# Kernel tuning notes

Hardware: AMD Instinct MI355X
Metric: run time of the kernel (lower is better)

Reference implementation:

```python
import jax, jax.numpy as jnp
import numpy as np
import math

IN_CH = 256
RED_CH = 32  # max(256//8, 32)

def setup_inputs() -> dict:
    key = jax.random.key(0)
    k1, k2, k3, k4, k5 = jax.random.split(key, 5)
    x = jax.random.normal(k1, (2, IN_CH, 8, 28, 28), dtype=jnp.float32)
    # 1x1x1 Conv3d weights, kaiming-normal style scale (fan_out)
    def kaiming(k, shape):
        fan_out = shape[0]
        std = math.sqrt(2.0 / fan_out)
        return jax.random.normal(k, shape, dtype=jnp.float32) * std
    q_w = kaiming(k2, (RED_CH, IN_CH))
    k_w = kaiming(k3, (RED_CH, IN_CH))
    v_w = kaiming(k4, (RED_CH, IN_CH))
    out_w = kaiming(k5, (IN_CH, RED_CH))
    return {"x": x, "q_w": q_w, "k_w": k_w, "v_w": v_w, "out_w": out_w}

def reference(x, q_w, k_w, v_w, out_w):
    b, c, t, h, w = x.shape
    n = t * h * w
    xf = x.reshape(b, c, n)  # [B, C, N] (1x1x1 conv == channel matmul)
    q = jnp.einsum('rc,bcn->brn', q_w, xf)  # [B, Cr, N]
    k = jnp.einsum('rc,bcn->brn', k_w, xf)
    v = jnp.einsum('rc,bcn->brn', v_w, xf)
    scale = 1.0 / math.sqrt(RED_CH)
    attn = jnp.einsum('bri,brj->bij', q, k) * scale  # [B, N, N]
    attn = jax.nn.softmax(attn, axis=2)
    out = jnp.einsum('brj,bij->bri', v, attn)  # [B, Cr, N]
    out = jnp.einsum('cr,brn->bcn', out_w, out).reshape(b, c, t, h, w)
    return x + out
```

## Files before the change

kernel.cpp:

```cpp
#include <hip/hip_runtime.h>
#include <hip/hip_bf16.h>

#define NPOS 6272
#define NT   98
#define CIN  256
#define CR   32
#define BATCH 2
#define QS2  0.25503371989518595f
#define PPITCH 72

typedef short bf16x8s __attribute__((ext_vector_type(8)));
typedef short short4v __attribute__((ext_vector_type(4)));
typedef float f32x4   __attribute__((ext_vector_type(4)));
typedef unsigned short ushort_t;

__device__ __forceinline__ ushort_t f2bf(float f) {
    unsigned u = __builtin_bit_cast(unsigned, f);
    u += 0x7fff + ((u >> 16) & 1);
    return (ushort_t)(u >> 16);
}
__device__ __forceinline__ float bf2f(ushort_t h) {
    return __builtin_bit_cast(float, (unsigned)h << 16);
}

__global__ __launch_bounds__(256) void qkv_kernel(
    const float* __restrict__ x, const float* __restrict__ qw,
    const float* __restrict__ kw, const float* __restrict__ vw,
    ushort_t* __restrict__ Qh, ushort_t* __restrict__ Ql,
    ushort_t* __restrict__ Kh, ushort_t* __restrict__ Kl,
    ushort_t* __restrict__ Vt)
{
    const int b   = blockIdx.y;
    const int z   = blockIdx.z;
    const int nl  = threadIdx.x & 63;
    const int n   = blockIdx.x * 64 + nl;
    const int g   = __builtin_amdgcn_readfirstlane(threadIdx.x >> 6);
    const float* w  = (z == 0) ? qw : (z == 1) ? kw : vw;
    const float* xb = x + (size_t)b * CIN * NPOS + n;

    float acc[8];
#pragma unroll
    for (int i = 0; i < 8; ++i) acc[i] = 0.f;
#pragma unroll 8
    for (int c = 0; c < CIN; ++c) {
        float xv = xb[(size_t)c * NPOS];
#pragma unroll
        for (int i = 0; i < 8; ++i)
            acc[i] += w[(g * 8 + i) * CIN + c] * xv;
    }
    if (z == 2) {
#pragma unroll
        for (int i = 0; i < 8; ++i)
            Vt[((size_t)b * CR + g * 8 + i) * NPOS + n] = f2bf(acc[i]);
    } else {
        ushort_t* dh = (z == 0) ? Qh : Kh;
        ushort_t* dl = (z == 0) ? Ql : Kl;
        float s = (z == 0) ? QS2 : 1.0f;
        bf16x8s fh, fl;
#pragma unroll
        for (int i = 0; i < 8; ++i) {
            float v = acc[i] * s;
            ushort_t h = f2bf(v);
            fh[i] = (short)h;
            fl[i] = (short)f2bf(v - bf2f(h));
        }
        size_t off = ((size_t)b * NPOS + n) * CR + g * 8;
        *(bf16x8s*)(dh + off) = fh;
        *(bf16x8s*)(dl + off) = fl;
    }
}

__device__ __forceinline__ void load_tile(
    const ushort_t* __restrict__ Khb, const ushort_t* __restrict__ Klb,
    const ushort_t* __restrict__ Vtb, int j0, int col, int quad,
    bf16x8s* kh, bf16x8s* kl, bf16x8s* vb)
{
#pragma unroll
    for (int f = 0; f < 4; ++f) {
        kh[f] = *(const bf16x8s*)(Khb + (size_t)(j0 + f * 16 + col) * CR + quad * 8);
        kl[f] = *(const bf16x8s*)(Klb + (size_t)(j0 + f * 16 + col) * CR + quad * 8);
    }
#pragma unroll
    for (int k2 = 0; k2 < 2; ++k2)
#pragma unroll
        for (int c = 0; c < 2; ++c)
            vb[k2 * 2 + c] = *(const bf16x8s*)(
                Vtb + (size_t)(c * 16 + col) * NPOS + j0 + k2 * 32 + quad * 8);
}

__device__ __forceinline__ void compute_tile(
    const bf16x8s* kh, const bf16x8s* kl, const bf16x8s* vb,
    const bf16x8s* qbh, const bf16x8s* qbl,
    f32x4 (&oc)[2][2], float (&m_)[2], float (&l_)[2],
    ushort_t* pb, int col, int quad)
{
    f32x4 z4 = {0.f, 0.f, 0.f, 0.f};
#pragma unroll
    for (int h = 0; h < 2; ++h) {
        f32x4 sc[4];
#pragma unroll
        for (int f = 0; f < 4; ++f) {
            sc[f] = __builtin_amdgcn_mfma_f32_16x16x32_bf16(kl[f], qbh[h], z4, 0, 0, 0);
            sc[f] = __builtin_amdgcn_mfma_f32_16x16x32_bf16(kh[f], qbl[h], sc[f], 0, 0, 0);
            sc[f] = __builtin_amdgcn_mfma_f32_16x16x32_bf16(kh[f], qbh[h], sc[f], 0, 0, 0);
        }
        float v0 = fmaxf(fmaxf(sc[0][0], sc[0][1]), fmaxf(sc[0][2], sc[0][3]));
        float v1 = fmaxf(fmaxf(sc[1][0], sc[1][1]), fmaxf(sc[1][2], sc[1][3]));
        float v2 = fmaxf(fmaxf(sc[2][0], sc[2][1]), fmaxf(sc[2][2], sc[2][3]));
        float v3 = fmaxf(fmaxf(sc[3][0], sc[3][1]), fmaxf(sc[3][2], sc[3][3]));
        float v  = fmaxf(fmaxf(v0, v1), fmaxf(v2, v3));
        v = fmaxf(v, __shfl_xor(v, 16));
        v = fmaxf(v, __shfl_xor(v, 32));
        float mo = m_[h];
        float mn = fmaxf(mo, v);
        float al = __builtin_amdgcn_exp2f(mo - mn);
        float lsum = 0.f;
#pragma unroll
        for (int f = 0; f < 4; ++f) {
            float p0 = __builtin_amdgcn_exp2f(sc[f][0] - mn);
            float p1 = __builtin_amdgcn_exp2f(sc[f][1] - mn);
            float p2 = __builtin_amdgcn_exp2f(sc[f][2] - mn);
            float p3 = __builtin_amdgcn_exp2f(sc[f][3] - mn);
            lsum += (p0 + p1) + (p2 + p3);
            short4v pk;
            pk[0] = (short)f2bf(p0); pk[1] = (short)f2bf(p1);
            pk[2] = (short)f2bf(p2); pk[3] = (short)f2bf(p3);
            *(short4v*)(&pb[h * 16 * PPITCH + col * PPITCH + f * 16 + quad * 4]) = pk;
        }
        m_[h] = mn;
        l_[h] = l_[h] * al + lsum;
#pragma unroll
        for (int r = 0; r < 4; ++r) { oc[h][0][r] *= al; oc[h][1][r] *= al; }
    }
#pragma unroll
    for (int h = 0; h < 2; ++h) {
#pragma unroll
        for (int k2 = 0; k2 < 2; ++k2) {
            bf16x8s pbo = *(const bf16x8s*)(
                &pb[h * 16 * PPITCH + col * PPITCH + k2 * 32 + quad * 8]);
            oc[h][0] = __builtin_amdgcn_mfma_f32_16x16x32_bf16(vb[k2 * 2 + 0], pbo, oc[h][0], 0, 0, 0);
            oc[h][1] = __builtin_amdgcn_mfma_f32_16x16x32_bf16(vb[k2 * 2 + 1], pbo, oc[h][1], 0, 0, 0);
        }
    }
}

template <int ITERS>
__global__ __launch_bounds__(128, 2) void attn_kernel(
    const ushort_t* __restrict__ Qh, const ushort_t* __restrict__ Ql,
    const ushort_t* __restrict__ Kh, const ushort_t* __restrict__ Kl,
    const ushort_t* __restrict__ Vt, ushort_t* __restrict__ Opart,
    float* __restrict__ Mp, float* __restrict__ Lp)
{
    __shared__ __align__(16) ushort_t pbuf[2 * 2 * 16 * PPITCH];

    const int lane = threadIdx.x & 63;
    const int wv   = threadIdx.x >> 6;
    const int col  = lane & 15;
    const int quad = lane >> 4;
    const int b    = blockIdx.z;
    const int s    = blockIdx.y;
    const int qw0  = blockIdx.x * 64 + wv * 32;
    ushort_t* pb   = &pbuf[wv * 2 * 16 * PPITCH];

    const ushort_t* Qhb = Qh + (size_t)b * NPOS * CR;
    const ushort_t* Qlb = Ql + (size_t)b * NPOS * CR;
    const ushort_t* Khb = Kh + (size_t)b * NPOS * CR;
    const ushort_t* Klb = Kl + (size_t)b * NPOS * CR;
    const ushort_t* Vtb = Vt + (size_t)b * CR * NPOS;

    bf16x8s qbh[2], qbl[2];
    qbh[0] = *(const bf16x8s*)(Qhb + (size_t)(qw0 + col) * CR + quad * 8);
    qbh[1] = *(const bf16x8s*)(Qhb + (size_t)(qw0 + 16 + col) * CR + quad * 8);
    qbl[0] = *(const bf16x8s*)(Qlb + (size_t)(qw0 + col) * CR + quad * 8);
    qbl[1] = *(const bf16x8s*)(Qlb + (size_t)(qw0 + 16 + col) * CR + quad * 8);

    f32x4 oc[2][2];
#pragma unroll
    for (int h = 0; h < 2; ++h)
#pragma unroll
        for (int c = 0; c < 2; ++c)
#pragma unroll
            for (int r = 0; r < 4; ++r) oc[h][c][r] = 0.f;
    float m_[2] = { -1e30f, -1e30f };
    float l_[2] = { 0.f, 0.f };

    if constexpr (ITERS <= 14) {
        bf16x8s ckh[4], ckl[4], cvb[4], nkh[4], nkl[4], nvb[4];
        load_tile(Khb, Klb, Vtb, s * ITERS * 64, col, quad, ckh, ckl, cvb);
#pragma unroll
        for (int it = 0; it < ITERS; ++it) {
            if (it + 1 < ITERS)
                load_tile(Khb, Klb, Vtb, (s * ITERS + it + 1) * 64, col, quad,
                          nkh, nkl, nvb);
            compute_tile(ckh, ckl, cvb, qbh, qbl, oc, m_, l_, pb, col, quad);
            if (it + 1 < ITERS) {
#pragma unroll
                for (int f = 0; f < 4; ++f) {
                    ckh[f] = nkh[f]; ckl[f] = nkl[f]; cvb[f] = nvb[f];
                }
            }
        }
    } else {
        for (int it = 0; it < ITERS; ++it) {
            bf16x8s kh[4], kl[4], vb[4];
            load_tile(Khb, Klb, Vtb, (s * ITERS + it) * 64, col, quad, kh, kl, vb);
            compute_tile(kh, kl, vb, qbh, qbl, oc, m_, l_, pb, col, quad);
        }
    }

#pragma unroll
    for (int h = 0; h < 2; ++h) {
        float l = l_[h];
        l += __shfl_xor(l, 16);
        l += __shfl_xor(l, 32);
        l_[h] = l;
    }

    const size_t sb = (size_t)(s * BATCH + b);
    ushort_t* Ob = Opart + sb * CR * NPOS;
#pragma unroll
    for (int h = 0; h < 2; ++h)
#pragma unroll
        for (int c = 0; c < 2; ++c)
#pragma unroll
            for (int r = 0; r < 4; ++r) {
                int ch = c * 16 + quad * 4 + r;
                Ob[(size_t)ch * NPOS + qw0 + h * 16 + col] = f2bf(oc[h][c][r]);
            }
    if (quad == 0) {
#pragma unroll
        for (int h = 0; h < 2; ++h) {
            Mp[sb * NPOS + qw0 + h * 16 + col] = m_[h];
            Lp[sb * NPOS + qw0 + h * 16 + col] = l_[h];
        }
    }
}

template <int S_>
__global__ __launch_bounds__(256) void merge_kernel(
    const ushort_t* __restrict__ Opart, const float* __restrict__ Mp,
    const float* __restrict__ Lp, float* __restrict__ Omrg)
{
    const int b  = blockIdx.y;
    const int z  = blockIdx.z;
    const int nl = threadIdx.x & 63;
    const int n  = blockIdx.x * 64 + nl;
    const int g  = __builtin_amdgcn_readfirstlane(threadIdx.x >> 6);
    const int r  = z * 4 + g;

    float mg = -1e30f;
#pragma unroll
    for (int s = 0; s < S_; ++s)
        mg = fmaxf(mg, Mp[(size_t)(s * BATCH + b) * NPOS + n]);
    float lg = 0.f, acc = 0.f;
#pragma unroll
    for (int s = 0; s < S_; ++s) {
        size_t sb = (size_t)(s * BATCH + b);
        float w = __builtin_amdgcn_exp2f(Mp[sb * NPOS + n] - mg);
        lg  += w * Lp[sb * NPOS + n];
        acc += w * bf2f(Opart[(sb * CR + r) * NPOS + n]);
    }
    Omrg[((size_t)b * CR + r) * NPOS + n] = acc / lg;
}

__global__ __launch_bounds__(256) void proj_kernel(
    const float* __restrict__ Omrg, const float* __restrict__ ow,
    const float* __restrict__ x, float* __restrict__ y)
{
    const int b  = blockIdx.y;
    const int z  = blockIdx.z;
    const int nl = threadIdx.x & 63;
    const int n  = blockIdx.x * 64 + nl;
    const int g  = __builtin_amdgcn_readfirstlane(threadIdx.x >> 6);

    float o[CR];
#pragma unroll
    for (int r = 0; r < CR; ++r)
        o[r] = Omrg[((size_t)b * CR + r) * NPOS + n];

    const float* xb = x + (size_t)b * CIN * NPOS + n;
    float*       yb = y + (size_t)b * CIN * NPOS + n;
    const int c0 = z * 32 + g * 8;
#pragma unroll
    for (int cc = 0; cc < 8; ++cc) {
        int c = c0 + cc;
        float acc = xb[(size_t)c * NPOS];
#pragma unroll
        for (int r = 0; r < CR; ++r) acc += ow[c * CR + r] * o[r];
        yb[(size_t)c * NPOS] = acc;
    }
}

extern "C" void kernel_launch(void* const* d_in, const int* in_sizes, int n_in,
                              void* d_out, int out_size, void* d_ws, size_t ws_size,
                              hipStream_t stream)
{
    const float* x  = (const float*)d_in[0];
    const float* qw = (const float*)d_in[1];
    const float* kw = (const float*)d_in[2];
    const float* vw = (const float*)d_in[3];
    const float* ow = (const float*)d_in[4];
    float* out = (float*)d_out;

    const size_t qkvN = (size_t)BATCH * CR * NPOS;
    const int s_cand[4] = {14, 7, 2, 1};
    int S = 1;
    for (int i = 0; i < 4; ++i) {
        int Sc = s_cand[i];
        size_t need = 5 * qkvN * sizeof(ushort_t)
                    + qkvN * sizeof(float)
                    + (size_t)Sc * qkvN * sizeof(ushort_t)
                    + 2 * (size_t)Sc * BATCH * NPOS * sizeof(float);
        if (need <= ws_size) { S = Sc; break; }
    }
    ushort_t* Qh = (ushort_t*)d_ws;
    ushort_t* Ql = Qh + qkvN;
    ushort_t* Kh = Ql + qkvN;
    ushort_t* Kl = Kh + qkvN;
    ushort_t* Vt = Kl + qkvN;
    float* Omrg  = (float*)(Vt + qkvN);
    ushort_t* Op = (ushort_t*)(Omrg + qkvN);
    float* Mp    = (float*)(Op + (size_t)S * qkvN);
    float* Lp    = Mp + (size_t)S * BATCH * NPOS;

    qkv_kernel<<<dim3(NT, BATCH, 3), 256, 0, stream>>>(x, qw, kw, vw,
                                                       Qh, Ql, Kh, Kl, Vt);
    dim3 ag(NT, S, BATCH);
    switch (S) {
        case 14: attn_kernel<7> <<<ag, 128, 0, stream>>>(Qh, Ql, Kh, Kl, Vt, Op, Mp, Lp); break;
        case 7:  attn_kernel<14><<<ag, 128, 0, stream>>>(Qh, Ql, Kh, Kl, Vt, Op, Mp, Lp); break;
        case 2:  attn_kernel<49><<<ag, 128, 0, stream>>>(Qh, Ql, Kh, Kl, Vt, Op, Mp, Lp); break;
        default: attn_kernel<98><<<ag, 128, 0, stream>>>(Qh, Ql, Kh, Kl, Vt, Op, Mp, Lp); break;
    }
    dim3 mg(NT, BATCH, 8);
    switch (S) {
        case 14: merge_kernel<14><<<mg, 256, 0, stream>>>(Op, Mp, Lp, Omrg); break;
        case 7:  merge_kernel<7> <<<mg, 256, 0, stream>>>(Op, Mp, Lp, Omrg); break;
        case 2:  merge_kernel<2> <<<mg, 256, 0, stream>>>(Op, Mp, Lp, Omrg); break;
        default: merge_kernel<1> <<<mg, 256, 0, stream>>>(Op, Mp, Lp, Omrg); break;
    }
    proj_kernel<<<dim3(NT, BATCH, 8), 256, 0, stream>>>(Omrg, ow, x, out);
}
```

Measured before the change: 144.3 us.

## Compute QKV projection with split-bf16 MFMA after a transposing prepass

Replaces the scalar FP32 QKV projection with a two-stage path. A prepass transposes x to position-major layout and splits x and the weights into bf16 high/low pairs. A second kernel then computes Q, K and V with three bf16 MFMAs per K-chunk to approximate FP32 accuracy. This trades the scalar FMA work for an extra kernel launch and an extra write and read of the split x tensor, and it slightly changes numerics by dropping the low*low term.

```diff
diff --git a/kernel.cpp b/kernel.cpp
--- a/kernel.cpp
+++ b/kernel.cpp
@@ -23,50 +23,112 @@
     return __builtin_bit_cast(float, (unsigned)h << 16);
 }
 
-__global__ __launch_bounds__(256) void qkv_kernel(
+__global__ __launch_bounds__(64) void prepass_kernel(
     const float* __restrict__ x, const float* __restrict__ qw,
     const float* __restrict__ kw, const float* __restrict__ vw,
+    ushort_t* __restrict__ xhT, ushort_t* __restrict__ xlT,
+    ushort_t* __restrict__ whs, ushort_t* __restrict__ wls)
+{
+    const int b = blockIdx.y;
+    const int z = blockIdx.z;
+    const int t = threadIdx.x;
+
+    if (z < 8) {
+        const int n  = blockIdx.x * 64 + t;
+        const int c0 = z * 32;
+        const float* xb = x + (size_t)b * CIN * NPOS + n;
+        ushort_t* dh = xhT + ((size_t)b * NPOS + n) * CIN + c0;
+        ushort_t* dl = xlT + ((size_t)b * NPOS + n) * CIN + c0;
+#pragma unroll
+        for (int blk = 0; blk < 4; ++blk) {
+            float v[8];
+#pragma unroll
+            for (int i = 0; i < 8; ++i)
+                v[i] = xb[(size_t)(c0 + blk * 8 + i) * NPOS];
+            bf16x8s fh, fl;
+#pragma unroll
+            for (int i = 0; i < 8; ++i) {
+                ushort_t h = f2bf(v[i]);
+                fh[i] = (short)h;
+                fl[i] = (short)f2bf(v[i] - bf2f(h));
+            }
+            *(bf16x8s*)(dh + blk * 8) = fh;
+            *(bf16x8s*)(dl + blk * 8) = fl;
+        }
+    } else {
+        const int tid = blockIdx.x * 2 + b;
+        if (tid >= 96) return;
+        const int m = tid >> 5;
+        const int r = tid & 31;
+        const float* w = (m == 0) ? qw : (m == 1) ? kw : vw;
+        const float  s = (m == 0) ? QS2 : 1.0f;
+        const int c0 = t * 4;
+        short4v hv, lv;
+#pragma unroll
+        for (int i = 0; i < 4; ++i) {
+            float v = w[r * CIN + c0 + i] * s;
+            ushort_t h = f2bf(v);
+            hv[i] = (short)h;
+            lv[i] = (short)f2bf(v - bf2f(h));
+        }
+        *(short4v*)(whs + ((size_t)m * CR + r) * CIN + c0) = hv;
+        *(short4v*)(wls + ((size_t)m * CR + r) * CIN + c0) = lv;
+    }
+}
+
+__global__ __launch_bounds__(64) void qkv_mfma_kernel(
+    const ushort_t* __restrict__ xhT, const ushort_t* __restrict__ xlT,
+    const ushort_t* __restrict__ whs, const ushort_t* __restrict__ wls,
     ushort_t* __restrict__ Qh, ushort_t* __restrict__ Ql,
     ushort_t* __restrict__ Kh, ushort_t* __restrict__ Kl,
     ushort_t* __restrict__ Vt)
 {
-    const int b   = blockIdx.y;
-    const int z   = blockIdx.z;
-    const int nl  = threadIdx.x & 63;
-    const int n   = blockIdx.x * 64 + nl;
-    const int g   = __builtin_amdgcn_readfirstlane(threadIdx.x >> 6);
-    const float* w  = (z == 0) ? qw : (z == 1) ? kw : vw;
-    const float* xb = x + (size_t)b * CIN * NPOS + n;
-
-    float acc[8];
-#pragma unroll
-    for (int i = 0; i < 8; ++i) acc[i] = 0.f;
-#pragma unroll 8
-    for (int c = 0; c < CIN; ++c) {
-        float xv = xb[(size_t)c * NPOS];
-#pragma unroll
-        for (int i = 0; i < 8; ++i)
-            acc[i] += w[(g * 8 + i) * CIN + c] * xv;
-    }
-    if (z == 2) {
-#pragma unroll
-        for (int i = 0; i < 8; ++i)
-            Vt[((size_t)b * CR + g * 8 + i) * NPOS + n] = f2bf(acc[i]);
+    const int lane = threadIdx.x;
+    const int col  = lane & 15;
+    const int quad = lane >> 4;
+    const int b    = blockIdx.y;
+    const int z    = blockIdx.z;
+    const int mat  = z >> 1;
+    const int rt   = z & 1;
+    const int p0   = blockIdx.x * 16;
+
+    const ushort_t* xh = xhT + ((size_t)b * NPOS + p0 + col) * CIN;
+    const ushort_t* xl = xlT + ((size_t)b * NPOS + p0 + col) * CIN;
+    const ushort_t* wh = whs + ((size_t)mat * CR + rt * 16 + col) * CIN;
+    const ushort_t* wl = wls + ((size_t)mat * CR + rt * 16 + col) * CIN;
+
+    f32x4 acc = {0.f, 0.f, 0.f, 0.f};
+#pragma unroll
+    for (int kc = 0; kc < 8; ++kc) {
+        const int off = kc * 32 + quad * 8;
+        bf16x8s ah = *(const bf16x8s*)(wh + off);
+        bf16x8s al = *(const bf16x8s*)(wl + off);
+        bf16x8s bh = *(const bf16x8s*)(xh + off);
+        bf16x8s bl = *(const bf16x8s*)(xl + off);
+        acc = __builtin_amdgcn_mfma_f32_16x16x32_bf16(ah, bh, acc, 0, 0, 0);
+        acc = __builtin_amdgcn_mfma_f32_16x16x32_bf16(ah, bl, acc, 0, 0, 0);
+        acc = __builtin_amdgcn_mfma_f32_16x16x32_bf16(al, bh, acc, 0, 0, 0);
+    }
+
+    if (mat < 2) {
+        ushort_t* dh = (mat == 0) ? Qh : Kh;
+        ushort_t* dl = (mat == 0) ? Ql : Kl;
+        short4v hv, lv;
+#pragma unroll
+        for (int r = 0; r < 4; ++r) {
+            float v = acc[r];
+            ushort_t h = f2bf(v);
+            hv[r] = (short)h;
+            lv[r] = (short)f2bf(v - bf2f(h));
+        }
+        size_t off = ((size_t)b * NPOS + p0 + col) * CR + rt * 16 + quad * 4;
+        *(short4v*)(dh + off) = hv;
+        *(short4v*)(dl + off) = lv;
     } else {
-        ushort_t* dh = (z == 0) ? Qh : Kh;
-        ushort_t* dl = (z == 0) ? Ql : Kl;
-        float s = (z == 0) ? QS2 : 1.0f;
-        bf16x8s fh, fl;
-#pragma unroll
-        for (int i = 0; i < 8; ++i) {
-            float v = acc[i] * s;
-            ushort_t h = f2bf(v);
-            fh[i] = (short)h;
-            fl[i] = (short)f2bf(v - bf2f(h));
-        }
-        size_t off = ((size_t)b * NPOS + n) * CR + g * 8;
-        *(bf16x8s*)(dh + off) = fh;
-        *(bf16x8s*)(dl + off) = fl;
+#pragma unroll
+        for (int r = 0; r < 4; ++r)
+            Vt[((size_t)b * CR + rt * 16 + quad * 4 + r) * NPOS + p0 + col] =
+                f2bf(acc[r]);
     }
 }
 
@@ -303,28 +365,36 @@
     float* out = (float*)d_out;
 
     const size_t qkvN = (size_t)BATCH * CR * NPOS;
+    const size_t xsz  = (size_t)BATCH * CIN * NPOS;
+    const size_t wsz  = (size_t)3 * CR * CIN;
     const int s_cand[4] = {14, 7, 2, 1};
     int S = 1;
     for (int i = 0; i < 4; ++i) {
         int Sc = s_cand[i];
-        size_t need = 5 * qkvN * sizeof(ushort_t)
+        size_t need = (2 * xsz + 2 * wsz + 5 * qkvN
+                       + (size_t)Sc * qkvN) * sizeof(ushort_t)
                     + qkvN * sizeof(float)
-                    + (size_t)Sc * qkvN * sizeof(ushort_t)
                     + 2 * (size_t)Sc * BATCH * NPOS * sizeof(float);
         if (need <= ws_size) { S = Sc; break; }
     }
-    ushort_t* Qh = (ushort_t*)d_ws;
-    ushort_t* Ql = Qh + qkvN;
-    ushort_t* Kh = Ql + qkvN;
-    ushort_t* Kl = Kh + qkvN;
-    ushort_t* Vt = Kl + qkvN;
-    float* Omrg  = (float*)(Vt + qkvN);
-    ushort_t* Op = (ushort_t*)(Omrg + qkvN);
-    float* Mp    = (float*)(Op + (size_t)S * qkvN);
-    float* Lp    = Mp + (size_t)S * BATCH * NPOS;
-
-    qkv_kernel<<<dim3(NT, BATCH, 3), 256, 0, stream>>>(x, qw, kw, vw,
-                                                       Qh, Ql, Kh, Kl, Vt);
+    ushort_t* xhT = (ushort_t*)d_ws;
+    ushort_t* xlT = xhT + xsz;
+    ushort_t* whs = xlT + xsz;
+    ushort_t* wls = whs + wsz;
+    ushort_t* Qh  = wls + wsz;
+    ushort_t* Ql  = Qh + qkvN;
+    ushort_t* Kh  = Ql + qkvN;
+    ushort_t* Kl  = Kh + qkvN;
+    ushort_t* Vt  = Kl + qkvN;
+    ushort_t* Op  = Vt + qkvN;
+    float* Omrg   = (float*)(Op + (size_t)S * qkvN);
+    float* Mp     = Omrg + qkvN;
+    float* Lp     = Mp + (size_t)S * BATCH * NPOS;
+
+    prepass_kernel<<<dim3(NT, BATCH, 9), 64, 0, stream>>>(
+        x, qw, kw, vw, xhT, xlT, whs, wls);
+    qkv_mfma_kernel<<<dim3(392, BATCH, 6), 64, 0, stream>>>(
+        xhT, xlT, whs, wls, Qh, Ql, Kh, Kl, Vt);
     dim3 ag(NT, S, BATCH);
     switch (S) {
         case 14: attn_kernel<7> <<<ag, 128, 0, stream>>>(Qh, Ql, Kh, Kl, Vt, Op, Mp, Lp); break;
```

New measurement: 151.6 us. 5.0% more time.

## Fuse merge and projection kernels and stage x tiles into LDS asynchronously

Applied to the files above, without the earlier changes.

Merge and output-projection now run as one kernel, so the fp32 merged-attention buffer is no longer written to global memory and read back, and one launch is removed. The merged 32-channel result is kept in LDS and each block computes all 256 output channels for its 64 positions. Both the QKV kernel and the fused kernel load the 64-position x tile into LDS with async global-to-LDS copies. The fused grid shrinks from 8x to 196 blocks, and each block now uses 72KB of LDS, which limits occupancy and parallelism.

```diff
diff --git a/kernel.cpp b/kernel.cpp
--- a/kernel.cpp
+++ b/kernel.cpp
@@ -23,6 +23,12 @@
     return __builtin_bit_cast(float, (unsigned)h << 16);
 }
 
+__device__ __forceinline__ void async_ld16(const float* g, float* l) {
+    __builtin_amdgcn_global_load_lds(
+        (const __attribute__((address_space(1))) void*)g,
+        (__attribute__((address_space(3))) void*)l, 16, 0, 0);
+}
+
 __global__ __launch_bounds__(256) void qkv_kernel(
     const float* __restrict__ x, const float* __restrict__ qw,
     const float* __restrict__ kw, const float* __restrict__ vw,
@@ -30,20 +36,31 @@
     ushort_t* __restrict__ Kh, ushort_t* __restrict__ Kl,
     ushort_t* __restrict__ Vt)
 {
+    __shared__ __align__(16) float lx[CIN * 64];
+
     const int b   = blockIdx.y;
     const int z   = blockIdx.z;
     const int nl  = threadIdx.x & 63;
-    const int n   = blockIdx.x * 64 + nl;
+    const int n0  = blockIdx.x * 64;
+    const int n   = n0 + nl;
     const int g   = __builtin_amdgcn_readfirstlane(threadIdx.x >> 6);
     const float* w  = (z == 0) ? qw : (z == 1) ? kw : vw;
-    const float* xb = x + (size_t)b * CIN * NPOS + n;
+    const float* xb = x + (size_t)b * CIN * NPOS + n0;
+
+#pragma unroll
+    for (int j = 0; j < 16; ++j) {
+        const int c0 = g * 64 + j * 4;
+        async_ld16(xb + (size_t)(c0 + (nl >> 4)) * NPOS + (nl & 15) * 4,
+                   &lx[c0 * 64]);
+    }
+    __syncthreads();
 
     float acc[8];
 #pragma unroll
     for (int i = 0; i < 8; ++i) acc[i] = 0.f;
 #pragma unroll 8
     for (int c = 0; c < CIN; ++c) {
-        float xv = xb[(size_t)c * NPOS];
+        float xv = lx[c * 64 + nl];
 #pragma unroll
         for (int i = 0; i < 8; ++i)
             acc[i] += w[(g * 8 + i) * CIN + c] * xv;
@@ -237,54 +254,63 @@
 }
 
 template <int S_>
-__global__ __launch_bounds__(256) void merge_kernel(
+__global__ __launch_bounds__(256) void mergeproj_kernel(
     const ushort_t* __restrict__ Opart, const float* __restrict__ Mp,
-    const float* __restrict__ Lp, float* __restrict__ Omrg)
-{
+    const float* __restrict__ Lp, const float* __restrict__ ow,
+    const float* __restrict__ x, float* __restrict__ y)
+{
+    __shared__ __align__(16) float lx[CIN * 64];
+    __shared__ float ox[CR * 64];
+
     const int b  = blockIdx.y;
-    const int z  = blockIdx.z;
     const int nl = threadIdx.x & 63;
-    const int n  = blockIdx.x * 64 + nl;
+    const int n0 = blockIdx.x * 64;
+    const int n  = n0 + nl;
     const int g  = __builtin_amdgcn_readfirstlane(threadIdx.x >> 6);
-    const int r  = z * 4 + g;
+    const float* xb = x + (size_t)b * CIN * NPOS + n0;
+
+#pragma unroll
+    for (int j = 0; j < 16; ++j) {
+        const int c0 = g * 64 + j * 4;
+        async_ld16(xb + (size_t)(c0 + (nl >> 4)) * NPOS + (nl & 15) * 4,
+                   &lx[c0 * 64]);
+    }
 
     float mg = -1e30f;
 #pragma unroll
     for (int s = 0; s < S_; ++s)
         mg = fmaxf(mg, Mp[(size_t)(s * BATCH + b) * NPOS + n]);
-    float lg = 0.f, acc = 0.f;
+    float wseg[S_];
+    float lg = 0.f;
 #pragma unroll
     for (int s = 0; s < S_; ++s) {
         size_t sb = (size_t)(s * BATCH + b);
         float w = __builtin_amdgcn_exp2f(Mp[sb * NPOS + n] - mg);
-        lg  += w * Lp[sb * NPOS + n];
-        acc += w * bf2f(Opart[(sb * CR + r) * NPOS + n]);
-    }
-    Omrg[((size_t)b * CR + r) * NPOS + n] = acc / lg;
-}
-
-__global__ __launch_bounds__(256) void proj_kernel(
-    const float* __restrict__ Omrg, const float* __restrict__ ow,
-    const float* __restrict__ x, float* __restrict__ y)
-{
-    const int b  = blockIdx.y;
-    const int z  = blockIdx.z;
-    const int nl = threadIdx.x & 63;
-    const int n  = blockIdx.x * 64 + nl;
-    const int g  = __builtin_amdgcn_readfirstlane(threadIdx.x >> 6);
+        wseg[s] = w;
+        lg += w * Lp[sb * NPOS + n];
+    }
+    float inv = 1.f / lg;
+#pragma unroll
+    for (int i = 0; i < 8; ++i) {
+        int r = g * 8 + i;
+        float acc = 0.f;
+#pragma unroll
+        for (int s = 0; s < S_; ++s)
+            acc += wseg[s] *
+                   bf2f(Opart[((size_t)(s * BATCH + b) * CR + r) * NPOS + n]);
+        ox[r * 64 + nl] = acc * inv;
+    }
+    __syncthreads();
 
     float o[CR];
 #pragma unroll
-    for (int r = 0; r < CR; ++r)
-        o[r] = Omrg[((size_t)b * CR + r) * NPOS + n];
-
-    const float* xb = x + (size_t)b * CIN * NPOS + n;
-    float*       yb = y + (size_t)b * CIN * NPOS + n;
-    const int c0 = z * 32 + g * 8;
-#pragma unroll
-    for (int cc = 0; cc < 8; ++cc) {
-        int c = c0 + cc;
-        float acc = xb[(size_t)c * NPOS];
+    for (int r = 0; r < CR; ++r) o[r] = ox[r * 64 + nl];
+
+    float* yb = y + (size_t)b * CIN * NPOS + n;
+#pragma unroll 2
+    for (int cc = 0; cc < 64; ++cc) {
+        int c = g * 64 + cc;
+        float acc = lx[c * 64 + nl];
 #pragma unroll
         for (int r = 0; r < CR; ++r) acc += ow[c * CR + r] * o[r];
         yb[(size_t)c * NPOS] = acc;
@@ -307,9 +333,7 @@
     int S = 1;
     for (int i = 0; i < 4; ++i) {
         int Sc = s_cand[i];
-        size_t need = 5 * qkvN * sizeof(ushort_t)
-                    + qkvN * sizeof(float)
-                    + (size_t)Sc * qkvN * sizeof(ushort_t)
+        size_t need = (5 * qkvN + (size_t)Sc * qkvN) * sizeof(ushort_t)
                     + 2 * (size_t)Sc * BATCH * NPOS * sizeof(float);
         if (need <= ws_size) { S = Sc; break; }
     }
@@ -318,8 +342,7 @@
     ushort_t* Kh = Ql + qkvN;
     ushort_t* Kl = Kh + qkvN;
     ushort_t* Vt = Kl + qkvN;
-    float* Omrg  = (float*)(Vt + qkvN);
-    ushort_t* Op = (ushort_t*)(Omrg + qkvN);
+    ushort_t* Op = Vt + qkvN;
     float* Mp    = (float*)(Op + (size_t)S * qkvN);
     float* Lp    = Mp + (size_t)S * BATCH * NPOS;
 
@@ -332,12 +355,11 @@
         case 2:  attn_kernel<49><<<ag, 128, 0, stream>>>(Qh, Ql, Kh, Kl, Vt, Op, Mp, Lp); break;
         default: attn_kernel<98><<<ag, 128, 0, stream>>>(Qh, Ql, Kh, Kl, Vt, Op, Mp, Lp); break;
     }
-    dim3 mg(NT, BATCH, 8);
+    dim3 mp(NT, BATCH);
     switch (S) {
-        case 14: merge_kernel<14><<<mg, 256, 0, stream>>>(Op, Mp, Lp, Omrg); break;
-        case 7:  merge_kernel<7> <<<mg, 256, 0, stream>>>(Op, Mp, Lp, Omrg); break;
-        case 2:  merge_kernel<2> <<<mg, 256, 0, stream>>>(Op, Mp, Lp, Omrg); break;
-        default: merge_kernel<1> <<<mg, 256, 0, stream>>>(Op, Mp, Lp, Omrg); break;
-    }
-    proj_kernel<<<dim3(NT, BATCH, 8), 256, 0, stream>>>(Omrg, ow, x, out);
-}
+        case 14: mergeproj_kernel<14><<<mp, 256, 0, stream>>>(Op, Mp, Lp, ow, x, out); break;
+        case 7:  mergeproj_kernel<7> <<<mp, 256, 0, stream>>>(Op, Mp, Lp, ow, x, out); break;
+        case 2:  mergeproj_kernel<2> <<<mp, 256, 0, stream>>>(Op, Mp, Lp, ow, x, out); break;
+        default: mergeproj_kernel<1> <<<mp, 256, 0, stream>>>(Op, Mp, Lp, ow, x, out); break;
+    }
+}
```

Measured after the change: 175.6 us. 1.22x slower.

## Precompute row max in a first pass to drop online softmax rescaling

Applied to the files above, without the earlier changes.

Adds a cheap first pass that computes an approximate per-query row max from the bf16-high K and Q parts over the split's key range. The main loop then uses this fixed max, which removes the per-tile max reduction, cross-lane shuffles, alpha exp and accumulator rescaling. It also double-buffers the P staging buffer in LDS, drops the explicit register prefetch of the next tile, raises the occupancy hint to 3 blocks per CU, and reorders workspace layout. The extra pass re-reads K and adds MFMAs, and the max taken from the high part only may differ slightly from the true max, which carries a small overflow risk.

```diff
diff --git a/kernel.cpp b/kernel.cpp
--- a/kernel.cpp
+++ b/kernel.cpp
@@ -8,6 +8,7 @@
 #define BATCH 2
 #define QS2  0.25503371989518595f
 #define PPITCH 72
+#define PBWAVE (2 * 16 * PPITCH)
 
 typedef short bf16x8s __attribute__((ext_vector_type(8)));
 typedef short short4v __attribute__((ext_vector_type(4)));
@@ -70,88 +71,14 @@
     }
 }
 
-__device__ __forceinline__ void load_tile(
-    const ushort_t* __restrict__ Khb, const ushort_t* __restrict__ Klb,
-    const ushort_t* __restrict__ Vtb, int j0, int col, int quad,
-    bf16x8s* kh, bf16x8s* kl, bf16x8s* vb)
-{
-#pragma unroll
-    for (int f = 0; f < 4; ++f) {
-        kh[f] = *(const bf16x8s*)(Khb + (size_t)(j0 + f * 16 + col) * CR + quad * 8);
-        kl[f] = *(const bf16x8s*)(Klb + (size_t)(j0 + f * 16 + col) * CR + quad * 8);
-    }
-#pragma unroll
-    for (int k2 = 0; k2 < 2; ++k2)
-#pragma unroll
-        for (int c = 0; c < 2; ++c)
-            vb[k2 * 2 + c] = *(const bf16x8s*)(
-                Vtb + (size_t)(c * 16 + col) * NPOS + j0 + k2 * 32 + quad * 8);
-}
-
-__device__ __forceinline__ void compute_tile(
-    const bf16x8s* kh, const bf16x8s* kl, const bf16x8s* vb,
-    const bf16x8s* qbh, const bf16x8s* qbl,
-    f32x4 (&oc)[2][2], float (&m_)[2], float (&l_)[2],
-    ushort_t* pb, int col, int quad)
-{
-    f32x4 z4 = {0.f, 0.f, 0.f, 0.f};
-#pragma unroll
-    for (int h = 0; h < 2; ++h) {
-        f32x4 sc[4];
-#pragma unroll
-        for (int f = 0; f < 4; ++f) {
-            sc[f] = __builtin_amdgcn_mfma_f32_16x16x32_bf16(kl[f], qbh[h], z4, 0, 0, 0);
-            sc[f] = __builtin_amdgcn_mfma_f32_16x16x32_bf16(kh[f], qbl[h], sc[f], 0, 0, 0);
-            sc[f] = __builtin_amdgcn_mfma_f32_16x16x32_bf16(kh[f], qbh[h], sc[f], 0, 0, 0);
-        }
-        float v0 = fmaxf(fmaxf(sc[0][0], sc[0][1]), fmaxf(sc[0][2], sc[0][3]));
-        float v1 = fmaxf(fmaxf(sc[1][0], sc[1][1]), fmaxf(sc[1][2], sc[1][3]));
-        float v2 = fmaxf(fmaxf(sc[2][0], sc[2][1]), fmaxf(sc[2][2], sc[2][3]));
-        float v3 = fmaxf(fmaxf(sc[3][0], sc[3][1]), fmaxf(sc[3][2], sc[3][3]));
-        float v  = fmaxf(fmaxf(v0, v1), fmaxf(v2, v3));
-        v = fmaxf(v, __shfl_xor(v, 16));
-        v = fmaxf(v, __shfl_xor(v, 32));
-        float mo = m_[h];
-        float mn = fmaxf(mo, v);
-        float al = __builtin_amdgcn_exp2f(mo - mn);
-        float lsum = 0.f;
-#pragma unroll
-        for (int f = 0; f < 4; ++f) {
-            float p0 = __builtin_amdgcn_exp2f(sc[f][0] - mn);
-            float p1 = __builtin_amdgcn_exp2f(sc[f][1] - mn);
-            float p2 = __builtin_amdgcn_exp2f(sc[f][2] - mn);
-            float p3 = __builtin_amdgcn_exp2f(sc[f][3] - mn);
-            lsum += (p0 + p1) + (p2 + p3);
-            short4v pk;
-            pk[0] = (short)f2bf(p0); pk[1] = (short)f2bf(p1);
-            pk[2] = (short)f2bf(p2); pk[3] = (short)f2bf(p3);
-            *(short4v*)(&pb[h * 16 * PPITCH + col * PPITCH + f * 16 + quad * 4]) = pk;
-        }
-        m_[h] = mn;
-        l_[h] = l_[h] * al + lsum;
-#pragma unroll
-        for (int r = 0; r < 4; ++r) { oc[h][0][r] *= al; oc[h][1][r] *= al; }
-    }
-#pragma unroll
-    for (int h = 0; h < 2; ++h) {
-#pragma unroll
-        for (int k2 = 0; k2 < 2; ++k2) {
-            bf16x8s pbo = *(const bf16x8s*)(
-                &pb[h * 16 * PPITCH + col * PPITCH + k2 * 32 + quad * 8]);
-            oc[h][0] = __builtin_amdgcn_mfma_f32_16x16x32_bf16(vb[k2 * 2 + 0], pbo, oc[h][0], 0, 0, 0);
-            oc[h][1] = __builtin_amdgcn_mfma_f32_16x16x32_bf16(vb[k2 * 2 + 1], pbo, oc[h][1], 0, 0, 0);
-        }
-    }
-}
-
 template <int ITERS>
-__global__ __launch_bounds__(128, 2) void attn_kernel(
+__global__ __launch_bounds__(128, 3) void attn_kernel(
     const ushort_t* __restrict__ Qh, const ushort_t* __restrict__ Ql,
     const ushort_t* __restrict__ Kh, const ushort_t* __restrict__ Kl,
     const ushort_t* __restrict__ Vt, ushort_t* __restrict__ Opart,
     float* __restrict__ Mp, float* __restrict__ Lp)
 {
-    __shared__ __align__(16) ushort_t pbuf[2 * 2 * 16 * PPITCH];
+    __shared__ __align__(16) ushort_t pbuf[2][2 * PBWAVE];
 
     const int lane = threadIdx.x & 63;
     const int wv   = threadIdx.x >> 6;
@@ -160,7 +87,6 @@
     const int b    = blockIdx.z;
     const int s    = blockIdx.y;
     const int qw0  = blockIdx.x * 64 + wv * 32;
-    ushort_t* pb   = &pbuf[wv * 2 * 16 * PPITCH];
 
     const ushort_t* Qhb = Qh + (size_t)b * NPOS * CR;
     const ushort_t* Qlb = Ql + (size_t)b * NPOS * CR;
@@ -174,6 +100,31 @@
     qbl[0] = *(const bf16x8s*)(Qlb + (size_t)(qw0 + col) * CR + quad * 8);
     qbl[1] = *(const bf16x8s*)(Qlb + (size_t)(qw0 + 16 + col) * CR + quad * 8);
 
+    const f32x4 z4 = {0.f, 0.f, 0.f, 0.f};
+
+    float mx[2] = { -1e30f, -1e30f };
+#pragma unroll
+    for (int it = 0; it < ITERS; ++it) {
+        const int j0 = (s * ITERS + it) * 64;
+        bf16x8s kh[4];
+#pragma unroll
+        for (int f = 0; f < 4; ++f)
+            kh[f] = *(const bf16x8s*)(Khb + (size_t)(j0 + f * 16 + col) * CR + quad * 8);
+#pragma unroll
+        for (int h = 0; h < 2; ++h) {
+#pragma unroll
+            for (int f = 0; f < 4; ++f) {
+                f32x4 sc = __builtin_amdgcn_mfma_f32_16x16x32_bf16(kh[f], qbh[h], z4, 0, 0, 0);
+                mx[h] = fmaxf(mx[h], fmaxf(fmaxf(sc[0], sc[1]), fmaxf(sc[2], sc[3])));
+            }
+        }
+    }
+#pragma unroll
+    for (int h = 0; h < 2; ++h) {
+        mx[h] = fmaxf(mx[h], __shfl_xor(mx[h], 16));
+        mx[h] = fmaxf(mx[h], __shfl_xor(mx[h], 32));
+    }
+
     f32x4 oc[2][2];
 #pragma unroll
     for (int h = 0; h < 2; ++h)
@@ -181,30 +132,59 @@
         for (int c = 0; c < 2; ++c)
 #pragma unroll
             for (int r = 0; r < 4; ++r) oc[h][c][r] = 0.f;
-    float m_[2] = { -1e30f, -1e30f };
     float l_[2] = { 0.f, 0.f };
 
-    if constexpr (ITERS <= 14) {
-        bf16x8s ckh[4], ckl[4], cvb[4], nkh[4], nkl[4], nvb[4];
-        load_tile(Khb, Klb, Vtb, s * ITERS * 64, col, quad, ckh, ckl, cvb);
-#pragma unroll
-        for (int it = 0; it < ITERS; ++it) {
-            if (it + 1 < ITERS)
-                load_tile(Khb, Klb, Vtb, (s * ITERS + it + 1) * 64, col, quad,
-                          nkh, nkl, nvb);
-            compute_tile(ckh, ckl, cvb, qbh, qbl, oc, m_, l_, pb, col, quad);
-            if (it + 1 < ITERS) {
-#pragma unroll
-                for (int f = 0; f < 4; ++f) {
-                    ckh[f] = nkh[f]; ckl[f] = nkl[f]; cvb[f] = nvb[f];
-                }
-            }
-        }
-    } else {
-        for (int it = 0; it < ITERS; ++it) {
-            bf16x8s kh[4], kl[4], vb[4];
-            load_tile(Khb, Klb, Vtb, (s * ITERS + it) * 64, col, quad, kh, kl, vb);
-            compute_tile(kh, kl, vb, qbh, qbl, oc, m_, l_, pb, col, quad);
+#pragma unroll
+    for (int it = 0; it < ITERS; ++it) {
+        const int j0 = (s * ITERS + it) * 64;
+        ushort_t* pb = &pbuf[it & 1][wv * PBWAVE];
+        bf16x8s kh[4], kl[4], vb[4];
+#pragma unroll
+        for (int f = 0; f < 4; ++f) {
+            kh[f] = *(const bf16x8s*)(Khb + (size_t)(j0 + f * 16 + col) * CR + quad * 8);
+            kl[f] = *(const bf16x8s*)(Klb + (size_t)(j0 + f * 16 + col) * CR + quad * 8);
+        }
+#pragma unroll
+        for (int k2 = 0; k2 < 2; ++k2)
+#pragma unroll
+            for (int c = 0; c < 2; ++c)
+                vb[k2 * 2 + c] = *(const bf16x8s*)(
+                    Vtb + (size_t)(c * 16 + col) * NPOS + j0 + k2 * 32 + quad * 8);
+
+#pragma unroll
+        for (int h = 0; h < 2; ++h) {
+            f32x4 sc[4];
+#pragma unroll
+            for (int f = 0; f < 4; ++f) {
+                sc[f] = __builtin_amdgcn_mfma_f32_16x16x32_bf16(kl[f], qbh[h], z4, 0, 0, 0);
+                sc[f] = __builtin_amdgcn_mfma_f32_16x16x32_bf16(kh[f], qbl[h], sc[f], 0, 0, 0);
+                sc[f] = __builtin_amdgcn_mfma_f32_16x16x32_bf16(kh[f], qbh[h], sc[f], 0, 0, 0);
+            }
+            const float mn = mx[h];
+            float lsum = 0.f;
+#pragma unroll
+            for (int f = 0; f < 4; ++f) {
+                float p0 = __builtin_amdgcn_exp2f(sc[f][0] - mn);
+                float p1 = __builtin_amdgcn_exp2f(sc[f][1] - mn);
+                float p2 = __builtin_amdgcn_exp2f(sc[f][2] - mn);
+                float p3 = __builtin_amdgcn_exp2f(sc[f][3] - mn);
+                lsum += (p0 + p1) + (p2 + p3);
+                short4v pk;
+                pk[0] = (short)f2bf(p0); pk[1] = (short)f2bf(p1);
+                pk[2] = (short)f2bf(p2); pk[3] = (short)f2bf(p3);
+                *(short4v*)(&pb[h * 16 * PPITCH + col * PPITCH + f * 16 + quad * 4]) = pk;
+            }
+            l_[h] += lsum;
+        }
+#pragma unroll
+        for (int h = 0; h < 2; ++h) {
+#pragma unroll
+            for (int k2 = 0; k2 < 2; ++k2) {
+                bf16x8s pbo = *(const bf16x8s*)(
+                    &pb[h * 16 * PPITCH + col * PPITCH + k2 * 32 + quad * 8]);
+                oc[h][0] = __builtin_amdgcn_mfma_f32_16x16x32_bf16(vb[k2 * 2 + 0], pbo, oc[h][0], 0, 0, 0);
+                oc[h][1] = __builtin_amdgcn_mfma_f32_16x16x32_bf16(vb[k2 * 2 + 1], pbo, oc[h][1], 0, 0, 0);
+            }
         }
     }
 
@@ -230,7 +210,7 @@
     if (quad == 0) {
 #pragma unroll
         for (int h = 0; h < 2; ++h) {
-            Mp[sb * NPOS + qw0 + h * 16 + col] = m_[h];
+            Mp[sb * NPOS + qw0 + h * 16 + col] = mx[h];
             Lp[sb * NPOS + qw0 + h * 16 + col] = l_[h];
         }
     }
@@ -307,9 +287,8 @@
     int S = 1;
     for (int i = 0; i < 4; ++i) {
         int Sc = s_cand[i];
-        size_t need = 5 * qkvN * sizeof(ushort_t)
+        size_t need = (5 * qkvN + (size_t)Sc * qkvN) * sizeof(ushort_t)
                     + qkvN * sizeof(float)
-                    + (size_t)Sc * qkvN * sizeof(ushort_t)
                     + 2 * (size_t)Sc * BATCH * NPOS * sizeof(float);
         if (need <= ws_size) { S = Sc; break; }
     }
@@ -318,9 +297,9 @@
     ushort_t* Kh = Ql + qkvN;
     ushort_t* Kl = Kh + qkvN;
     ushort_t* Vt = Kl + qkvN;
-    float* Omrg  = (float*)(Vt + qkvN);
-    ushort_t* Op = (ushort_t*)(Omrg + qkvN);
-    float* Mp    = (float*)(Op + (size_t)S * qkvN);
+    ushort_t* Op = Vt + qkvN;
+    float* Omrg  = (float*)(Op + (size_t)S * qkvN);
+    float* Mp    = Omrg + qkvN;
     float* Lp    = Mp + (size_t)S * BATCH * NPOS;
 
     qkv_kernel<<<dim3(NT, BATCH, 3), 256, 0, stream>>>(x, qw, kw, vw,
```

Measured after the change: 162.5 us. 1.13x slower.
